# Kernel optimization log

Hardware: AMD Instinct MI355X
Metric: run time of the kernel (lower is better)

## Reference

```python
import jax, jax.numpy as jnp
import numpy as np

B, N, F_IN, OUT_FEATS, NUM_CLS, NUM_INDS = 256, 200, 200, 256, 8, 512
PCT_EDGES = 20
K = int(PCT_EDGES / 100 * N * (N - 1) / 2)  # 3980 hard edges
TAU = 1.0


def setup_inputs() -> dict:
    key = jax.random.key(0)
    ks = jax.random.split(key, 6)
    x = jax.random.normal(ks[0], (B, N, F_IN), dtype=jnp.float32)
    gumbel_u = jax.random.uniform(ks[1], (B, N, N), dtype=jnp.float32)
    nets = jax.random.normal(ks[2], (NUM_INDS, N, N), dtype=jnp.float32)
    w_gnn = jax.random.normal(ks[3], (F_IN, OUT_FEATS), dtype=jnp.float32) / np.sqrt(F_IN).astype(np.float32)
    w_lin = jax.random.normal(ks[4], (OUT_FEATS, NUM_CLS), dtype=jnp.float32) / np.sqrt(OUT_FEATS).astype(np.float32)
    b_lin = jnp.zeros((NUM_CLS,), dtype=jnp.float32)
    net_index = jax.random.randint(ks[5], (B,), 0, NUM_INDS)
    return {"x": x, "gumbel_u": gumbel_u, "nets": nets, "w_gnn": w_gnn,
            "w_lin": w_lin, "b_lin": b_lin, "net_index": net_index}


def _gumbel_softkmax(logits, u, k, tau):
    # logits: [B, N, N]; u: uniform(0,1) noise -> Gumbel(0,1) via -log(-log(u))
    b, n, _ = logits.shape
    g = -jnp.log(-jnp.log(jnp.clip(u, 1e-10, 1.0 - 1e-10)))
    g = (logits + g) / tau
    sym = (g + jnp.swapaxes(g, 1, 2)) * 0.5                      # symmetrize
    y_soft = jax.nn.softmax(sym.reshape(b, -1), axis=-1).reshape(b, n, n)
    upper_flat = jnp.triu(y_soft).reshape(b, -1)                 # upper tri incl. diag
    _, idx = jax.lax.top_k(upper_flat, k)                        # [B, k]
    y_hard = jnp.zeros_like(upper_flat).at[jnp.arange(b)[:, None], idx].set(1.0)
    y_hard = y_hard.reshape(b, n, n)
    diag = jnp.diagonal(y_hard, axis1=-2, axis2=-1)              # [B, N]
    eye = jnp.eye(n, dtype=y_hard.dtype)
    y_hard = y_hard + jnp.swapaxes(y_hard, 1, 2) - diag[:, :, None] * eye
    # straight-through estimator
    return y_hard - jax.lax.stop_gradient(y_soft) + y_soft


def reference(x, gumbel_u, nets, w_gnn, w_lin, b_lin, net_index):
    selected = nets[net_index]                                   # [B, N, N]
    adj = _gumbel_softkmax(selected, gumbel_u, K, TAU)
    # gnn: relu(adj @ x @ W_gnn)  -> embeddings [B, N, OUT_FEATS]
    emb = jax.nn.relu(jnp.einsum('bij,bjf,fo->bio', adj, x, w_gnn))
    out = emb @ w_lin + b_lin                                    # [B, N, NUM_CLS]
    return out, emb, adj
```

## Files before the change

### kernel.cpp

```cpp
#include <hip/hip_runtime.h>
#include <math.h>

#define B_SZ 256
#define N_SZ 200
#define NN (N_SZ * N_SZ)
#define FIN 200
#define OUT_F 256
#define NCLS 8
#define KSEL 3980
#define NUPPER 20100
#define KSTRIDE 20128
#define NT 7
#define NTILES 28

#define ADJ_STRIDE 224
#define KGRP_PB 25
#define XWM_PB (KGRP_PB * 2048)

#define EMB_OFF (B_SZ * N_SZ * NCLS)
#define ADJ_OFF (EMB_OFF + B_SZ * N_SZ * OUT_F)

#define KEYS_OFF_B   0
#define WKG_OFF_B    26214400
#define ADJB16_OFF_B 26329088

typedef unsigned short ushort_t;
typedef float f32x4 __attribute__((ext_vector_type(4)));
typedef short bf16x8 __attribute__((ext_vector_type(8)));
typedef ushort_t u16x4 __attribute__((ext_vector_type(4)));
typedef ushort_t u16x8 __attribute__((ext_vector_type(8)));

__device__ __forceinline__ unsigned sortkey(float f) {
    unsigned u = __float_as_uint(f);
    return (u & 0x80000000u) ? ~u : (u | 0x80000000u);
}

__device__ __forceinline__ ushort_t f2b(float f) {
    unsigned u = __float_as_uint(f);
    return (ushort_t)((u + 0x7FFFu + ((u >> 16) & 1u)) >> 16);
}

__device__ __forceinline__ bf16x8 f2b8(float4 lo, float4 hi) {
    bf16x8 r;
    r[0] = (short)f2b(lo.x); r[1] = (short)f2b(lo.y);
    r[2] = (short)f2b(lo.z); r[3] = (short)f2b(lo.w);
    r[4] = (short)f2b(hi.x); r[5] = (short)f2b(hi.y);
    r[6] = (short)f2b(hi.z); r[7] = (short)f2b(hi.w);
    return r;
}

__device__ __forceinline__ void tile_decode(int t, int& ti, int& tj) {
    int a = 0, rem = t;
    while (rem >= NT - a) { rem -= NT - a; ++a; }
    ti = a; tj = a + rem;
}

__device__ __forceinline__ int rowbase(int i) {
    return i * N_SZ - (i * (i - 1)) / 2;
}

__global__ __launch_bounds__(256) void kA(
    const float* __restrict__ gu, const float* __restrict__ nets,
    const int* __restrict__ net_index, unsigned* __restrict__ keys,
    const float* __restrict__ wg, ushort_t* __restrict__ wkg)
{
    const int blk = blockIdx.x;
    if (blk >= B_SZ * NTILES) {
        int pb = blk - B_SZ * NTILES;
        int e = pb * 256 + threadIdx.x;
        int kg = e >> 11;
        int rem = e & 2047;
        int n = rem >> 3;
        int ki = rem & 7;
        int k = kg * 8 + ki;
        wkg[e] = (k < FIN) ? f2b(wg[k * OUT_F + n]) : (ushort_t)0;
        return;
    }
    const int b = blk / NTILES;
    int ti, tj; tile_decode(blk % NTILES, ti, tj);
    const int i0 = ti * 32, j0 = tj * 32;
    const float* ub = gu + (size_t)b * NN;
    const float* lb = nets + (size_t)net_index[b] * NN;

    __shared__ float Hij[32][33];
    __shared__ float Hji[32][33];

    const int r = threadIdx.x >> 5;
    const int c = threadIdx.x & 31;

    #pragma unroll
    for (int s = 0; s < 4; ++s) {
        int rr = r + 8 * s;
        int i = i0 + rr, j = j0 + c;
        if (i < N_SZ && j < N_SZ) {
            float u = ub[i * N_SZ + j];
            u = fminf(fmaxf(u, 1e-10f), 1.0f - 1e-10f);
            Hij[rr][c] = lb[i * N_SZ + j] - logf(-logf(u));
        }
        if (ti != tj) {
            int i2 = j0 + rr, j2 = i0 + c;
            if (i2 < N_SZ && j2 < N_SZ) {
                float u = ub[i2 * N_SZ + j2];
                u = fminf(fmaxf(u, 1e-10f), 1.0f - 1e-10f);
                Hji[rr][c] = lb[i2 * N_SZ + j2] - logf(-logf(u));
            }
        }
    }
    __syncthreads();

    unsigned* kb = keys + (size_t)b * KSTRIDE;
    #pragma unroll
    for (int s = 0; s < 4; ++s) {
        int rr = r + 8 * s;
        int i = i0 + rr, j = j0 + c;
        if (i < N_SZ && j < N_SZ && i <= j) {
            float hji = (ti == tj) ? Hij[c][rr] : Hji[c][rr];
            float sv = 0.5f * ((Hij[rr][c]) + hji);
            int base = i * N_SZ - (i * (i - 1)) / 2;
            kb[base + (j - i)] = sortkey(sv);
        }
    }
}

__global__ __launch_bounds__(1024) void kSelW(
    const unsigned* __restrict__ keys, float* __restrict__ out_base,
    ushort_t* __restrict__ adjb16)
{
    const int b = blockIdx.x;
    const int tid = threadIdx.x;
    __shared__ __align__(16) unsigned kl[NUPPER];
    __shared__ unsigned hist[256];
    __shared__ unsigned sfx[256];
    __shared__ unsigned scanA[1024];
    __shared__ unsigned M[N_SZ][7];
    __shared__ unsigned sPrefix;
    __shared__ int sKK;

    {
        const int4* kb4 = (const int4*)(keys + (size_t)b * KSTRIDE);
        int4* kl4 = (int4*)kl;
        for (int q = tid; q < 5025; q += 1024) kl4[q] = kb4[q];
    }
    for (int q = tid; q < N_SZ * 7; q += 1024) ((unsigned*)M)[q] = 0;

    unsigned prefix = 0;
    int kk = KSEL;
    for (int round = 0; round < 4; ++round) {
        const int shift = 24 - 8 * round;
        if (tid < 256) hist[tid] = 0;
        __syncthreads();
        for (int idx = tid; idx < NUPPER; idx += 1024) {
            unsigned key = kl[idx];
            bool in = (round == 0) || ((key >> (shift + 8)) == prefix);
            if (in) atomicAdd(&hist[(key >> shift) & 255u], 1u);
        }
        __syncthreads();
        if (tid < 256) sfx[tid] = hist[tid];
        __syncthreads();
        #pragma unroll
        for (int off = 1; off < 256; off <<= 1) {
            unsigned add = 0;
            if (tid < 256 && tid + off < 256) add = sfx[tid + off];
            __syncthreads();
            if (tid < 256) sfx[tid] += add;
            __syncthreads();
        }
        if (tid < 256) {
            unsigned above = (tid < 255) ? sfx[tid + 1] : 0u;
            if (sfx[tid] >= (unsigned)kk && above < (unsigned)kk) {
                sPrefix = (prefix << 8) | (unsigned)tid;
                sKK = kk - (int)above;
            }
        }
        __syncthreads();
        prefix = sPrefix;
        kk = sKK;
        __syncthreads();
    }
    const unsigned kth = prefix;

    const int lo = tid * 20;
    const int hi = (lo + 20 < NUPPER) ? lo + 20 : NUPPER;
    unsigned mycnt = 0;
    for (int idx = lo; idx < hi; ++idx)
        if (kl[idx] == kth) ++mycnt;
    scanA[tid] = mycnt;
    __syncthreads();
    #pragma unroll
    for (int off = 1; off < 1024; off <<= 1) {
        unsigned add = (tid >= off) ? scanA[tid - off] : 0u;
        __syncthreads();
        scanA[tid] += add;
        __syncthreads();
    }
    unsigned rank = scanA[tid] - mycnt;

    if (lo < NUPPER) {
        int iLo = 0, iHi = N_SZ - 1;
        while (iLo < iHi) {
            int mid = (iLo + iHi + 1) >> 1;
            if (rowbase(mid) <= lo) iLo = mid; else iHi = mid - 1;
        }
        int i = iLo;
        int nextBase = rowbase(i + 1);
        for (int idx = lo; idx < hi; ++idx) {
            while (idx >= nextBase) { ++i; nextBase = rowbase(i + 1); }
            unsigned key = kl[idx];
            bool dec;
            if (key > kth) dec = true;
            else if (key == kth) { dec = (rank < (unsigned)kk); ++rank; }
            else dec = false;
            if (dec) {
                int j = i + (idx - rowbase(i));
                atomicOr(&M[i][j >> 5], 1u << (j & 31));
                atomicOr(&M[j][i >> 5], 1u << (i & 31));
            }
        }
    }
    __syncthreads();

    float* adj = out_base + ADJ_OFF + (size_t)b * NN;
    for (int e = tid; e < 10000; e += 1024) {
        int i = e / 50;
        int j0 = (e % 50) * 4;
        unsigned wbits = M[i][j0 >> 5] >> (j0 & 31);
        float4 v;
        v.x = (wbits & 1u) ? 1.0f : 0.0f;
        v.y = (wbits & 2u) ? 1.0f : 0.0f;
        v.z = (wbits & 4u) ? 1.0f : 0.0f;
        v.w = (wbits & 8u) ? 1.0f : 0.0f;
        *(float4*)(adj + (size_t)i * N_SZ + j0) = v;
    }
    ushort_t* ab = adjb16 + (size_t)b * (N_SZ * ADJ_STRIDE);
    for (int e = tid; e < 5600; e += 1024) {
        int i = e / 28;
        int j0 = (e % 28) * 8;
        unsigned wbits = (j0 < N_SZ) ? (M[i][j0 >> 5] >> (j0 & 31)) : 0u;
        u16x8 v;
        #pragma unroll
        for (int q = 0; q < 8; ++q) {
            int j = j0 + q;
            v[q] = (j < N_SZ && (wbits & (1u << q))) ? (ushort_t)0x3F80 : (ushort_t)0;
        }
        *(u16x8*)(ab + (size_t)i * ADJ_STRIDE + j0) = v;
    }
}

__global__ __launch_bounds__(256) void k2_mfma(
    const float* __restrict__ x, const ushort_t* __restrict__ wkg,
    ushort_t* __restrict__ xwm)
{
    const int r0 = blockIdx.x * 64;
    const int tid = threadIdx.x;
    const int w = tid >> 6;
    const int l = tid & 63;
    const int g = l >> 4;
    const int r = l & 15;

    __shared__ __align__(16) ushort_t Cs[64 * 256];

    f32x4 acc[4][4];
    #pragma unroll
    for (int mf = 0; mf < 4; ++mf)
        #pragma unroll
        for (int nf = 0; nf < 4; ++nf)
            acc[mf][nf] = (f32x4){0.f, 0.f, 0.f, 0.f};

    for (int c = 0; c < 7; ++c) {
        const int koff = (c * 32 + g * 8 < FIN) ? (c * 32 + g * 8) : 0;
        bf16x8 af[4], bf[4];
        #pragma unroll
        for (int mf = 0; mf < 4; ++mf) {
            const float* ap = x + (size_t)(r0 + mf * 16 + r) * FIN + koff;
            float4 lo = *(const float4*)ap;
            float4 hi = *(const float4*)(ap + 4);
            af[mf] = f2b8(lo, hi);
        }
        #pragma unroll
        for (int nf = 0; nf < 4; ++nf)
            bf[nf] = *(const bf16x8*)(wkg + c * 8192 + g * 2048 + (w * 64 + nf * 16 + r) * 8);
        #pragma unroll
        for (int mf = 0; mf < 4; ++mf)
            #pragma unroll
            for (int nf = 0; nf < 4; ++nf)
                acc[mf][nf] = __builtin_amdgcn_mfma_f32_16x16x32_bf16(
                    af[mf], bf[nf], acc[mf][nf], 0, 0, 0);
    }

    #pragma unroll
    for (int mf = 0; mf < 4; ++mf) {
        #pragma unroll
        for (int jj = 0; jj < 4; ++jj) {
            int row = mf * 16 + g * 4 + jj;
            #pragma unroll
            for (int nf = 0; nf < 4; ++nf) {
                int col = w * 64 + nf * 16 + r;
                Cs[((row >> 3) << 11) + col * 8 + (row & 7)] = f2b(acc[mf][nf][jj]);
            }
        }
    }
    __syncthreads();
    #pragma unroll
    for (int kg = 0; kg < 8; ++kg) {
        int grow0 = r0 + kg * 8;
        int bb = grow0 / N_SZ;
        int jb = grow0 % N_SZ;
        ushort_t* dst = xwm + (size_t)bb * XWM_PB + ((jb >> 3) << 11);
        *(int4*)(dst + tid * 8) = *(const int4*)(Cs + (kg << 11) + tid * 8);
    }
}

__global__ __launch_bounds__(256) void k3_fused(
    const ushort_t* __restrict__ adjb16, const ushort_t* __restrict__ xwm,
    const float* __restrict__ wl, const float* __restrict__ bl,
    float* __restrict__ out_base)
{
    const int blk = blockIdx.x;
    const int xcd = blk & 7;
    const int idx = blk >> 3;
    const int b = xcd + 8 * (idx / 13);
    const int mt = idx % 13;
    const int tid = threadIdx.x;
    const int w = tid >> 6;
    const int l = tid & 63;
    const int g = l >> 4;
    const int r = l & 15;

    const ushort_t* adjb = adjb16 + (size_t)b * (N_SZ * ADJ_STRIDE);
    const ushort_t* xwb = xwm + (size_t)b * XWM_PB;

    __shared__ __align__(16) float Es[16 * 256];
    float (*red)[4][4][8] = (float(*)[4][4][8])Es;

    int arow = mt * 16 + r; if (arow > N_SZ - 1) arow = N_SZ - 1;
    bf16x8 aa[7];
    #pragma unroll
    for (int c = 0; c < 7; ++c)
        aa[c] = *(const bf16x8*)(adjb + arow * ADJ_STRIDE + c * 32 + g * 8);

    f32x4 acc[4];
    #pragma unroll
    for (int nf = 0; nf < 4; ++nf) acc[nf] = (f32x4){0.f, 0.f, 0.f, 0.f};

    #pragma unroll
    for (int c = 0; c < 7; ++c) {
        bf16x8 bf[4];
        #pragma unroll
        for (int nf = 0; nf < 4; ++nf)
            bf[nf] = *(const bf16x8*)(xwb + c * 8192 + g * 2048 + (w * 64 + nf * 16 + r) * 8);
        #pragma unroll
        for (int nf = 0; nf < 4; ++nf)
            acc[nf] = __builtin_amdgcn_mfma_f32_16x16x32_bf16(
                aa[c], bf[nf], acc[nf], 0, 0, 0);
    }

    #pragma unroll
    for (int j = 0; j < 4; ++j) {
        int rowl = g * 4 + j;
        #pragma unroll
        for (int nf = 0; nf < 4; ++nf)
            Es[rowl * 256 + w * 64 + nf * 16 + r] = fmaxf(acc[nf][j], 0.0f);
    }
    __syncthreads();
    #pragma unroll
    for (int q = 0; q < 4; ++q) {
        int e = q * 256 + tid;
        int rowl = e >> 6;
        int c4 = e & 63;
        int grow = mt * 16 + rowl;
        if (grow < N_SZ) {
            float4 v = *(const float4*)(Es + rowl * 256 + c4 * 4);
            *(float4*)(out_base + EMB_OFF + ((size_t)b * N_SZ + grow) * OUT_F + c4 * 4) = v;
        }
    }
    __syncthreads();

    float wlv[4][NCLS];
    #pragma unroll
    for (int nf = 0; nf < 4; ++nf) {
        int col = w * 64 + nf * 16 + r;
        #pragma unroll
        for (int cls = 0; cls < NCLS; ++cls) wlv[nf][cls] = wl[col * NCLS + cls];
    }
    #pragma unroll
    for (int j = 0; j < 4; ++j) {
        float e0 = fmaxf(acc[0][j], 0.0f);
        float e1 = fmaxf(acc[1][j], 0.0f);
        float e2 = fmaxf(acc[2][j], 0.0f);
        float e3 = fmaxf(acc[3][j], 0.0f);
        float pr[NCLS];
        #pragma unroll
        for (int cls = 0; cls < NCLS; ++cls)
            pr[cls] = e0 * wlv[0][cls] + e1 * wlv[1][cls]
                    + e2 * wlv[2][cls] + e3 * wlv[3][cls];
        #pragma unroll
        for (int off = 1; off <= 8; off <<= 1) {
            #pragma unroll
            for (int cls = 0; cls < NCLS; ++cls)
                pr[cls] += __shfl_xor(pr[cls], off, 64);
        }
        if (r < NCLS) red[w][g][j][r] = pr[r];
    }
    __syncthreads();

    if (tid < 16 * NCLS) {
        int rowl = tid >> 3, cls = tid & 7;
        int gg = rowl >> 2, jj = rowl & 3;
        int grow = mt * 16 + rowl;
        if (grow < N_SZ) {
            float s = red[0][gg][jj][cls] + red[1][gg][jj][cls]
                    + red[2][gg][jj][cls] + red[3][gg][jj][cls] + bl[cls];
            out_base[((size_t)b * N_SZ + grow) * NCLS + cls] = s;
        }
    }
}

extern "C" void kernel_launch(void* const* d_in, const int* in_sizes, int n_in,
                              void* d_out, int out_size, void* d_ws, size_t ws_size,
                              hipStream_t stream) {
    const float* x    = (const float*)d_in[0];
    const float* gu   = (const float*)d_in[1];
    const float* nets = (const float*)d_in[2];
    const float* wg   = (const float*)d_in[3];
    const float* wl   = (const float*)d_in[4];
    const float* bl   = (const float*)d_in[5];
    const int*   nidx = (const int*)d_in[6];
    float* out = (float*)d_out;

    char* ws = (char*)d_ws;
    unsigned* keys    = (unsigned*)(ws + KEYS_OFF_B);
    ushort_t* xwm     = (ushort_t*)(ws + KEYS_OFF_B);
    ushort_t* wkg     = (ushort_t*)(ws + WKG_OFF_B);
    ushort_t* adjb16  = (ushort_t*)(ws + ADJB16_OFF_B);

    kA<<<B_SZ * NTILES + 224, 256, 0, stream>>>(gu, nets, nidx, keys, wg, wkg);
    kSelW<<<B_SZ, 1024, 0, stream>>>(keys, out, adjb16);
    k2_mfma<<<(B_SZ * N_SZ) / 64, 256, 0, stream>>>(x, wkg, xwm);
    k3_fused<<<B_SZ * 13, 256, 0, stream>>>(adjb16, xwm, wl, bl, out);
}
```

Baseline: 139.1 us.

## Fuse Gumbel key generation into per-batch top-k selection kernel

```diff
diff --git a/kernel.cpp b/kernel.cpp
--- a/kernel.cpp
+++ b/kernel.cpp
@@ -9,7 +9,6 @@
 #define NCLS 8
 #define KSEL 3980
 #define NUPPER 20100
-#define KSTRIDE 20128
 #define NT 7
 #define NTILES 28
 
@@ -20,14 +19,12 @@
 #define EMB_OFF (B_SZ * N_SZ * NCLS)
 #define ADJ_OFF (EMB_OFF + B_SZ * N_SZ * OUT_F)
 
-#define KEYS_OFF_B   0
 #define WKG_OFF_B    26214400
 #define ADJB16_OFF_B 26329088
 
 typedef unsigned short ushort_t;
 typedef float f32x4 __attribute__((ext_vector_type(4)));
 typedef short bf16x8 __attribute__((ext_vector_type(8)));
-typedef ushort_t u16x4 __attribute__((ext_vector_type(4)));
 typedef ushort_t u16x8 __attribute__((ext_vector_type(8)));
 
 __device__ __forceinline__ unsigned sortkey(float f) {
@@ -59,15 +56,16 @@
     return i * N_SZ - (i * (i - 1)) / 2;
 }
 
-__global__ __launch_bounds__(256) void kA(
+__global__ __launch_bounds__(1024) void kAS(
     const float* __restrict__ gu, const float* __restrict__ nets,
-    const int* __restrict__ net_index, unsigned* __restrict__ keys,
-    const float* __restrict__ wg, ushort_t* __restrict__ wkg)
+    const int* __restrict__ net_index, const float* __restrict__ wg,
+    ushort_t* __restrict__ wkg, float* __restrict__ out_base,
+    ushort_t* __restrict__ adjb16)
 {
     const int blk = blockIdx.x;
-    if (blk >= B_SZ * NTILES) {
-        int pb = blk - B_SZ * NTILES;
-        int e = pb * 256 + threadIdx.x;
+    const int tid = threadIdx.x;
+    if (blk >= B_SZ) {
+        int e = (blk - B_SZ) * 1024 + tid;
         int kg = e >> 11;
         int rem = e & 2047;
         int n = rem >> 3;
@@ -76,59 +74,11 @@
         wkg[e] = (k < FIN) ? f2b(wg[k * OUT_F + n]) : (ushort_t)0;
         return;
     }
-    const int b = blk / NTILES;
-    int ti, tj; tile_decode(blk % NTILES, ti, tj);
-    const int i0 = ti * 32, j0 = tj * 32;
-    const float* ub = gu + (size_t)b * NN;
-    const float* lb = nets + (size_t)net_index[b] * NN;
-
+    const int b = blk;
+
+    __shared__ __align__(16) unsigned kl[NUPPER];
     __shared__ float Hij[32][33];
     __shared__ float Hji[32][33];
-
-    const int r = threadIdx.x >> 5;
-    const int c = threadIdx.x & 31;
-
-    #pragma unroll
-    for (int s = 0; s < 4; ++s) {
-        int rr = r + 8 * s;
-        int i = i0 + rr, j = j0 + c;
-        if (i < N_SZ && j < N_SZ) {
-            float u = ub[i * N_SZ + j];
-            u = fminf(fmaxf(u, 1e-10f), 1.0f - 1e-10f);
-            Hij[rr][c] = lb[i * N_SZ + j] - logf(-logf(u));
-        }
-        if (ti != tj) {
-            int i2 = j0 + rr, j2 = i0 + c;
-            if (i2 < N_SZ && j2 < N_SZ) {
-                float u = ub[i2 * N_SZ + j2];
-                u = fminf(fmaxf(u, 1e-10f), 1.0f - 1e-10f);
-                Hji[rr][c] = lb[i2 * N_SZ + j2] - logf(-logf(u));
-            }
-        }
-    }
-    __syncthreads();
-
-    unsigned* kb = keys + (size_t)b * KSTRIDE;
-    #pragma unroll
-    for (int s = 0; s < 4; ++s) {
-        int rr = r + 8 * s;
-        int i = i0 + rr, j = j0 + c;
-        if (i < N_SZ && j < N_SZ && i <= j) {
-            float hji = (ti == tj) ? Hij[c][rr] : Hji[c][rr];
-            float sv = 0.5f * ((Hij[rr][c]) + hji);
-            int base = i * N_SZ - (i * (i - 1)) / 2;
-            kb[base + (j - i)] = sortkey(sv);
-        }
-    }
-}
-
-__global__ __launch_bounds__(1024) void kSelW(
-    const unsigned* __restrict__ keys, float* __restrict__ out_base,
-    ushort_t* __restrict__ adjb16)
-{
-    const int b = blockIdx.x;
-    const int tid = threadIdx.x;
-    __shared__ __align__(16) unsigned kl[NUPPER];
     __shared__ unsigned hist[256];
     __shared__ unsigned sfx[256];
     __shared__ unsigned scanA[1024];
@@ -136,10 +86,40 @@
     __shared__ unsigned sPrefix;
     __shared__ int sKK;
 
-    {
-        const int4* kb4 = (const int4*)(keys + (size_t)b * KSTRIDE);
-        int4* kl4 = (int4*)kl;
-        for (int q = tid; q < 5025; q += 1024) kl4[q] = kb4[q];
+    const float* ub = gu + (size_t)b * NN;
+    const float* lb = nets + (size_t)net_index[b] * NN;
+
+    const int rr = tid >> 5;
+    const int cc = tid & 31;
+    for (int t = 0; t < NTILES; ++t) {
+        int ti, tj; tile_decode(t, ti, tj);
+        const int i0 = ti * 32, j0 = tj * 32;
+        {
+            int i = i0 + rr, j = j0 + cc;
+            if (i < N_SZ && j < N_SZ) {
+                float u = ub[i * N_SZ + j];
+                u = fminf(fmaxf(u, 1e-10f), 1.0f - 1e-10f);
+                Hij[rr][cc] = lb[i * N_SZ + j] - logf(-logf(u));
+            }
+            if (ti != tj) {
+                int i2 = j0 + rr, j2 = i0 + cc;
+                if (i2 < N_SZ && j2 < N_SZ) {
+                    float u = ub[i2 * N_SZ + j2];
+                    u = fminf(fmaxf(u, 1e-10f), 1.0f - 1e-10f);
+                    Hji[rr][cc] = lb[i2 * N_SZ + j2] - logf(-logf(u));
+                }
+            }
+        }
+        __syncthreads();
+        {
+            int i = i0 + rr, j = j0 + cc;
+            if (i < N_SZ && j < N_SZ && i <= j) {
+                float hji = (ti == tj) ? Hij[cc][rr] : Hji[cc][rr];
+                float sv = 0.5f * ((Hij[rr][cc]) + hji);
+                kl[rowbase(i) + (j - i)] = sortkey(sv);
+            }
+        }
+        __syncthreads();
     }
     for (int q = tid; q < N_SZ * 7; q += 1024) ((unsigned*)M)[q] = 0;
 
@@ -428,13 +408,11 @@
     float* out = (float*)d_out;
 
     char* ws = (char*)d_ws;
-    unsigned* keys    = (unsigned*)(ws + KEYS_OFF_B);
-    ushort_t* xwm     = (ushort_t*)(ws + KEYS_OFF_B);
+    ushort_t* xwm     = (ushort_t*)ws;
     ushort_t* wkg     = (ushort_t*)(ws + WKG_OFF_B);
     ushort_t* adjb16  = (ushort_t*)(ws + ADJB16_OFF_B);
 
-    kA<<<B_SZ * NTILES + 224, 256, 0, stream>>>(gu, nets, nidx, keys, wg, wkg);
-    kSelW<<<B_SZ, 1024, 0, stream>>>(keys, out, adjb16);
+    kAS<<<B_SZ + 56, 1024, 0, stream>>>(gu, nets, nidx, wg, wkg, out, adjb16);
     k2_mfma<<<(B_SZ * N_SZ) / 64, 256, 0, stream>>>(x, wkg, xwm);
     k3_fused<<<B_SZ * 13, 256, 0, stream>>>(adjb16, xwm, wl, bl, out);
 }
```

After: 143.8 us. +3.3%, slower.
